# Performance work log

Hardware: AMD Instinct MI355X
Metric: run time of the kernel (lower is better)

## Reference

```python
import jax, jax.numpy as jnp
import numpy as np

DIM = 384
HEAD_DIM = 32
NUM_HEADS = DIM // HEAD_DIM
SCALE = HEAD_DIM ** -0.5


def setup_inputs() -> dict:
    key = jax.random.key(0)
    k1, k2, k3, k4 = jax.random.split(key, 4)
    x = jax.random.normal(k1, (8, DIM, 32, 32), dtype=jnp.float32)
    # torch nn.Linear stores weight as [out_features, in_features]
    W_qkv = jax.random.normal(k2, (3 * DIM, DIM), dtype=jnp.float32) * (DIM ** -0.5)
    W_proj = jax.random.normal(k3, (DIM, DIM), dtype=jnp.float32) * (DIM ** -0.5)
    b_proj = jax.random.normal(k4, (DIM,), dtype=jnp.float32) * 0.01
    return {"x": x, "W_qkv": W_qkv, "W_proj": W_proj, "b_proj": b_proj}


def reference(x, W_qkv, W_proj, b_proj):
    B, C, H, W = x.shape
    N = H * W
    # flatten spatial -> tokens: (B, N, C)
    xt = x.reshape(B, C, N).transpose(0, 2, 1)
    # qkv projection (no bias): (B, N, 3C)
    qkv = jnp.einsum('bnc,oc->bno', xt, W_qkv)
    qkv = qkv.reshape(B, N, 3, NUM_HEADS, HEAD_DIM).transpose(2, 0, 3, 1, 4)
    q, k, v = qkv[0], qkv[1], qkv[2]  # each (B, h, N, d)
    attn = jnp.einsum('bhnd,bhmd->bhnm', q * SCALE, k)  # (B, h, N, N)
    attn = jax.nn.softmax(attn, axis=-1)
    out = jnp.einsum('bhnm,bhmd->bhnd', attn, v)  # (B, h, N, d)
    out = out.transpose(0, 2, 1, 3).reshape(B, N, C)
    out = jnp.einsum('bnc,oc->bno', out, W_proj) + b_proj
    # back to (B, C, H, W)
    return out.transpose(0, 2, 1).reshape(B, C, H, W)
```

## Files before the change

kernel.cpp:

```cpp
#include <hip/hip_runtime.h>
#include <hip/hip_bf16.h>

#define DIM   384
#define HD    32
#define NH    12
#define NT    1024
#define BATCH 8
#define C2 0.2550347244197545f
#define M2 11.541560327111707f


typedef short shortx8 __attribute__((ext_vector_type(8)));
typedef float floatx4 __attribute__((ext_vector_type(4)));

#define GLD_LDS(gp, lp) \
    __builtin_amdgcn_global_load_lds((__attribute__((address_space(1))) const void*)(gp), \
                                     (__attribute__((address_space(3))) void*)(lp), 16, 0, 0)

static __device__ __forceinline__ unsigned short f2bf(float f) {
    unsigned int u = __float_as_uint(f);
    u += 0x7fffu + ((u >> 16) & 1u);
    return (unsigned short)(u >> 16);
}

template <int NA, int NB>
static __device__ __forceinline__ void ldfrag(shortx8 (&A)[NA], shortx8 (&B)[NB],
                                              const unsigned short* ab,
                                              const unsigned short* bb, int ks) {
#pragma unroll
    for (int s = 0; s < NA; s++) A[s] = *(const shortx8*)(ab + s * 6144 + ks * 512);
#pragma unroll
    for (int s = 0; s < NB; s++) B[s] = *(const shortx8*)(bb + s * 6144 + ks * 512);
}
template <int NA, int NB>
static __device__ __forceinline__ void mmblk(floatx4 (&acc)[NA][NB],
                                             const shortx8 (&A)[NA], const shortx8 (&B)[NB]) {
#pragma unroll
    for (int sm = 0; sm < NA; sm++)
#pragma unroll
        for (int sn = 0; sn < NB; sn++)
            acc[sm][sn] = __builtin_amdgcn_mfma_f32_16x16x32_bf16(A[sm], B[sn], acc[sm][sn], 0, 0, 0);
}

__global__ __launch_bounds__(256) void k_pre(const float* __restrict__ x,
                                             const float* __restrict__ wq,
                                             const float* __restrict__ wp,
                                             unsigned short* __restrict__ xtf,
                                             unsigned short* __restrict__ wqf,
                                             unsigned short* __restrict__ wpf) {
    const int bid = blockIdx.x;
    if (bid < 3072) {
        __shared__ float t[32][33];
        const int xb_ = bid & 31, kstep = (bid >> 5) % 12, b = bid / 384;
        const int n0 = xb_ * 32;
        const int tid = threadIdx.x;
        const int row = tid >> 3, col4 = (tid & 7) * 4;
        const float* xb = x + ((size_t)b * DIM + kstep * 32) * NT + n0;
        const float4 v4 = *(const float4*)(xb + (size_t)row * NT + col4);
        t[row][col4 + 0] = v4.x;
        t[row][col4 + 1] = v4.y;
        t[row][col4 + 2] = v4.z;
        t[row][col4 + 3] = v4.w;
        __syncthreads();
        const int mtl = tid >> 7, kq = (tid >> 5) & 3, rem = tid & 31;
        const int mrow = rem >> 1, krH = rem & 1;
        ushort4 p;
        p.x = f2bf(t[kq * 8 + krH * 4 + 0][mtl * 16 + mrow]);
        p.y = f2bf(t[kq * 8 + krH * 4 + 1][mtl * 16 + mrow]);
        p.z = f2bf(t[kq * 8 + krH * 4 + 2][mtl * 16 + mrow]);
        p.w = f2bf(t[kq * 8 + krH * 4 + 3][mtl * 16 + mrow]);
        const size_t mtile = ((size_t)b * 1024 + n0) / 16 + mtl;
        const size_t off = ((mtile * 12 + kstep) * 4 + kq) * 128 + mrow * 8 + krH * 4;
        *(ushort4*)(xtf + off) = p;
    } else {
        const int tid = (bid - 3072) * 256 + threadIdx.x;
        const float* src; unsigned short* dst; int ci;
        if (tid < 110592) { ci = tid; src = wq; dst = wqf; }
        else              { ci = tid - 110592; src = wp; dst = wpf; }
        const int krH = ci & 1, orow = (ci >> 1) & 15, quad = (ci >> 5) & 3;
        const int t2 = ci >> 7, kstep = t2 % 12, ntile = t2 / 12;
        const int row = ntile * 16 + orow, col = kstep * 32 + quad * 8 + krH * 4;
        const float4 v = *(const float4*)(src + (size_t)row * DIM + col);
        ushort4 p;
        p.x = f2bf(v.x); p.y = f2bf(v.y); p.z = f2bf(v.z); p.w = f2bf(v.w);
        *(ushort4*)(dst + (size_t)ci * 4) = p;
    }
}

__global__ __launch_bounds__(256, 6) void k_qkv(const unsigned short* __restrict__ xtf,
                                                const unsigned short* __restrict__ wqf,
                                                unsigned short* __restrict__ qb,
                                                unsigned short* __restrict__ kvf) {
    const int lane = threadIdx.x & 63, w = threadIdx.x >> 6;
    const int quad = lane >> 4, l16 = lane & 15;
    const int m0 = blockIdx.x * 64 + (w & 1) * 32;
    const int n0 = blockIdx.y * 96 + (w >> 1) * 48;
    floatx4 acc[2][3] = {};
    const unsigned short* abase = xtf + ((size_t)(m0 >> 4) * 48 + quad) * 128 + l16 * 8;
    const unsigned short* bbase = wqf + ((size_t)(n0 >> 4) * 48 + quad) * 128 + l16 * 8;
    shortx8 A0[2], B0[3], A1[2], B1[3];
    ldfrag(A0, B0, abase, bbase, 0);
#pragma unroll
    for (int ks = 0; ks < 12; ks += 2) {
        if (ks + 1 < 12) ldfrag(A1, B1, abase, bbase, ks + 1);
        mmblk(acc, A0, B0);
        if (ks + 2 < 12) ldfrag(A0, B0, abase, bbase, ks + 2);
        mmblk(acc, A1, B1);
    }
    const int bi = m0 >> 10;
#pragma unroll
    for (int sn = 0; sn < 3; sn++) {
        const int o = n0 + sn * 16 + l16;
        const int which = (o >= 2 * DIM) ? 2 : (o >= DIM ? 1 : 0);
        const int rem = o - which * DIM;
        const int h = rem >> 5, d = rem & 31;
        const size_t hi = (size_t)bi * NH + h;
#pragma unroll
        for (int sm = 0; sm < 2; sm++) {
            if (which == 2) {
                const int nb = m0 + sm * 16 + quad * 4;
                const int n_ = nb & 1023;
                const int f = 2 + (d >> 4);
                const int ln = (d & 15) + 16 * ((n_ & 31) >> 3);
                ushort4 p;
                p.x = f2bf(acc[sm][sn][0]);
                p.y = f2bf(acc[sm][sn][1]);
                p.z = f2bf(acc[sm][sn][2]);
                p.w = f2bf(acc[sm][sn][3]);
                *(ushort4*)(kvf + ((hi * 32 + (n_ >> 5)) * 4 + f) * 512 + ln * 8 + (n_ & 7)) = p;
            } else {
#pragma unroll
                for (int r = 0; r < 4; r++) {
                    const int n = (m0 + sm * 16 + quad * 4 + r) & 1023;
                    const unsigned short val = f2bf(acc[sm][sn][r]);
                    if (which == 0) {
                        qb[(hi * NT + n) * HD + d] = val;
                    } else {
                        const int key = n & 31;
                        const int kf_ = ((key & 7) < 4) ? 0 : 1;
                        const int kk = key - 4 * kf_;
                        const int l16p = ((kk >> 3) << 2) | (kk & 3);
                        const int pos = (l16p + 16 * (d >> 3)) * 8 + (d & 7);
                        kvf[((hi * 32 + (n >> 5)) * 4 + kf_) * 512 + pos] = val;
                    }
                }
            }
        }
    }
}

__global__ __launch_bounds__(256, 6) void k_attn(const unsigned short* __restrict__ qb,
                                                 const unsigned short* __restrict__ kvf,
                                                 unsigned short* __restrict__ aoutf) {
    __shared__ __align__(16) unsigned short frag[2][2][4][512];
    const int lane = threadIdx.x & 63, w = threadIdx.x >> 6;
    const int quad = lane >> 4, l16 = lane & 15;
    const int g = blockIdx.x & 7, j = blockIdx.x >> 3;
    const int hi = g * 12 + j % 12;
    const int q0 = (j / 12) * 64 + w * 16;
    const unsigned short* Q = qb + (size_t)hi * NT * HD;

    const shortx8 qf = *(const shortx8*)(Q + (size_t)(q0 + l16) * HD + quad * 8);
    const unsigned short* gsrc = kvf + ((size_t)hi * 32 * 4 + w) * 512 + lane * 8;
    const int gstep = 4 * 512;

    const shortx8 ones = {16256, 16256, 16256, 16256, 16256, 16256, 16256, 16256};
    floatx4 olo = {}, ohi = {}, ds = {};
    const floatx4 zero = {};

#pragma unroll
    for (int t = 0; t < 2; t++)
        GLD_LDS(gsrc + (size_t)t * gstep, &frag[0][t][w][0]);
    __syncthreads();

    for (int p = 0; p < 16; p++) {
        const int pb = p & 1;
        if (p < 15) {
#pragma unroll
            for (int t = 0; t < 2; t++)
                GLD_LDS(gsrc + (size_t)((p + 1) * 2 + t) * gstep, &frag[pb ^ 1][t][w][0]);
        }
#pragma unroll
        for (int t = 0; t < 2; t++) {
            const unsigned short* fb = &frag[pb][t][0][0];
            const shortx8 kf0 = *(const shortx8*)(fb + 0 * 512 + lane * 8);
            const shortx8 kf1 = *(const shortx8*)(fb + 1 * 512 + lane * 8);
            const shortx8 vlo = *(const shortx8*)(fb + 2 * 512 + lane * 8);
            const shortx8 vhi = *(const shortx8*)(fb + 3 * 512 + lane * 8);
            const floatx4 s0 = __builtin_amdgcn_mfma_f32_16x16x32_bf16(kf0, qf, zero, 0, 0, 0);
            const floatx4 s1 = __builtin_amdgcn_mfma_f32_16x16x32_bf16(kf1, qf, zero, 0, 0, 0);
            float e[8];
#pragma unroll
            for (int r = 0; r < 4; r++) {
                e[r]     = __builtin_amdgcn_exp2f(fmaf(s0[r], C2, -M2));
                e[4 + r] = __builtin_amdgcn_exp2f(fmaf(s1[r], C2, -M2));
            }
            union { shortx8 s8; __hip_bfloat162 h[4]; } pk;
#pragma unroll
            for (int i = 0; i < 4; i++)
                pk.h[i] = __float22bfloat162_rn(make_float2(e[2 * i], e[2 * i + 1]));
            olo = __builtin_amdgcn_mfma_f32_16x16x32_bf16(pk.s8, vlo, olo, 0, 0, 0);
            ohi = __builtin_amdgcn_mfma_f32_16x16x32_bf16(pk.s8, vhi, ohi, 0, 0, 0);
            ds  = __builtin_amdgcn_mfma_f32_16x16x32_bf16(pk.s8, ones, ds, 0, 0, 0);
        }
        __syncthreads();
    }
    const int bi = hi / NH, h = hi % NH;
    const size_t mt0 = (size_t)bi * 64 + (q0 >> 4);
    const int kqlo = l16 >> 3, kr = l16 & 7;
    unsigned short* pp = aoutf + (mt0 * 12 + h) * 512 + kr;
#pragma unroll
    for (int r = 0; r < 4; r++) {
        const int mrow8 = (quad * 4 + r) * 8;
        const float inv = 1.0f / ds[r];
        pp[kqlo * 128 + mrow8]       = f2bf(olo[r] * inv);
        pp[(2 + kqlo) * 128 + mrow8] = f2bf(ohi[r] * inv);
    }
}

__global__ __launch_bounds__(256, 6) void k_proj(const unsigned short* __restrict__ aoutf,
                                                 const unsigned short* __restrict__ wpf,
                                                 const float* __restrict__ bias,
                                                 float* __restrict__ out) {
    const int lane = threadIdx.x & 63, w = threadIdx.x >> 6;
    const int quad = lane >> 4, l16 = lane & 15;
    const int m0 = blockIdx.x * 32 + (w & 1) * 16;
    const int n0 = blockIdx.y * 64 + (w >> 1) * 32;
    floatx4 acc[1][2] = {};
    const unsigned short* abase = aoutf + ((size_t)(m0 >> 4) * 48 + quad) * 128 + l16 * 8;
    const unsigned short* bbase = wpf + ((size_t)(n0 >> 4) * 48 + quad) * 128 + l16 * 8;
    shortx8 A0[1], B0[2], A1[1], B1[2];
    ldfrag(A0, B0, abase, bbase, 0);
#pragma unroll
    for (int ks = 0; ks < 12; ks += 2) {
        if (ks + 1 < 12) ldfrag(A1, B1, abase, bbase, ks + 1);
        mmblk(acc, A0, B0);
        if (ks + 2 < 12) ldfrag(A0, B0, abase, bbase, ks + 2);
        mmblk(acc, A1, B1);
    }
    const int bi = m0 >> 10;
#pragma unroll
    for (int sn = 0; sn < 2; sn++) {
        const int o = n0 + sn * 16 + l16;
        const float bv = bias[o];
        float* orow = out + ((size_t)bi * DIM + o) * NT;
        const int nb = (m0 + quad * 4) & 1023;
        float4 pack;
        pack.x = acc[0][sn][0] + bv;
        pack.y = acc[0][sn][1] + bv;
        pack.z = acc[0][sn][2] + bv;
        pack.w = acc[0][sn][3] + bv;
        *(float4*)(orow + nb) = pack;
    }
}

extern "C" void kernel_launch(void* const* d_in, const int* in_sizes, int n_in,
                              void* d_out, int out_size, void* d_ws, size_t ws_size,
                              hipStream_t stream) {
    const float* x     = (const float*)d_in[0];
    const float* wqkv  = (const float*)d_in[1];
    const float* wproj = (const float*)d_in[2];
    const float* bias  = (const float*)d_in[3];
    float* out = (float*)d_out;

    unsigned short* xtf  = (unsigned short*)d_ws;
    unsigned short* qb   = xtf + 3145728;
    unsigned short* kvf  = qb + 3145728;
    unsigned short* wqf  = kvf + 6291456;
    unsigned short* wpf  = wqf + 442368;
    unsigned short* aoutf = xtf;

    k_pre<<<3648, 256, 0, stream>>>(x, wqkv, wproj, xtf, wqf, wpf);
    k_qkv<<<dim3(128, 12), 256, 0, stream>>>(xtf, wqf, qb, kvf);
    k_attn<<<1536, 256, 0, stream>>>(qb, kvf, aoutf);
    k_proj<<<dim3(256, 6), 256, 0, stream>>>(aoutf, wpf, bias, out);
}
```

Baseline: 124.2 us.

## Fuse fp32-to-bf16 conversion into QKV and projection GEMMs, drop pre-pass kernel

```diff
diff --git a/kernel.cpp b/kernel.cpp
--- a/kernel.cpp
+++ b/kernel.cpp
@@ -23,126 +23,105 @@
     return (unsigned short)(u >> 16);
 }
 
-template <int NA, int NB>
-static __device__ __forceinline__ void ldfrag(shortx8 (&A)[NA], shortx8 (&B)[NB],
-                                              const unsigned short* ab,
-                                              const unsigned short* bb, int ks) {
-#pragma unroll
-    for (int s = 0; s < NA; s++) A[s] = *(const shortx8*)(ab + s * 6144 + ks * 512);
-#pragma unroll
-    for (int s = 0; s < NB; s++) B[s] = *(const shortx8*)(bb + s * 6144 + ks * 512);
-}
-template <int NA, int NB>
-static __device__ __forceinline__ void mmblk(floatx4 (&acc)[NA][NB],
-                                             const shortx8 (&A)[NA], const shortx8 (&B)[NB]) {
-#pragma unroll
-    for (int sm = 0; sm < NA; sm++)
-#pragma unroll
-        for (int sn = 0; sn < NB; sn++)
-            acc[sm][sn] = __builtin_amdgcn_mfma_f32_16x16x32_bf16(A[sm], B[sn], acc[sm][sn], 0, 0, 0);
-}
-
-__global__ __launch_bounds__(256) void k_pre(const float* __restrict__ x,
-                                             const float* __restrict__ wq,
-                                             const float* __restrict__ wp,
-                                             unsigned short* __restrict__ xtf,
-                                             unsigned short* __restrict__ wqf,
-                                             unsigned short* __restrict__ wpf) {
-    const int bid = blockIdx.x;
-    if (bid < 3072) {
-        __shared__ float t[32][33];
-        const int xb_ = bid & 31, kstep = (bid >> 5) % 12, b = bid / 384;
-        const int n0 = xb_ * 32;
-        const int tid = threadIdx.x;
-        const int row = tid >> 3, col4 = (tid & 7) * 4;
-        const float* xb = x + ((size_t)b * DIM + kstep * 32) * NT + n0;
-        const float4 v4 = *(const float4*)(xb + (size_t)row * NT + col4);
-        t[row][col4 + 0] = v4.x;
-        t[row][col4 + 1] = v4.y;
-        t[row][col4 + 2] = v4.z;
-        t[row][col4 + 3] = v4.w;
-        __syncthreads();
-        const int mtl = tid >> 7, kq = (tid >> 5) & 3, rem = tid & 31;
-        const int mrow = rem >> 1, krH = rem & 1;
-        ushort4 p;
-        p.x = f2bf(t[kq * 8 + krH * 4 + 0][mtl * 16 + mrow]);
-        p.y = f2bf(t[kq * 8 + krH * 4 + 1][mtl * 16 + mrow]);
-        p.z = f2bf(t[kq * 8 + krH * 4 + 2][mtl * 16 + mrow]);
-        p.w = f2bf(t[kq * 8 + krH * 4 + 3][mtl * 16 + mrow]);
-        const size_t mtile = ((size_t)b * 1024 + n0) / 16 + mtl;
-        const size_t off = ((mtile * 12 + kstep) * 4 + kq) * 128 + mrow * 8 + krH * 4;
-        *(ushort4*)(xtf + off) = p;
-    } else {
-        const int tid = (bid - 3072) * 256 + threadIdx.x;
-        const float* src; unsigned short* dst; int ci;
-        if (tid < 110592) { ci = tid; src = wq; dst = wqf; }
-        else              { ci = tid - 110592; src = wp; dst = wpf; }
-        const int krH = ci & 1, orow = (ci >> 1) & 15, quad = (ci >> 5) & 3;
-        const int t2 = ci >> 7, kstep = t2 % 12, ntile = t2 / 12;
-        const int row = ntile * 16 + orow, col = kstep * 32 + quad * 8 + krH * 4;
-        const float4 v = *(const float4*)(src + (size_t)row * DIM + col);
-        ushort4 p;
-        p.x = f2bf(v.x); p.y = f2bf(v.y); p.z = f2bf(v.z); p.w = f2bf(v.w);
-        *(ushort4*)(dst + (size_t)ci * 4) = p;
-    }
-}
-
-__global__ __launch_bounds__(256, 6) void k_qkv(const unsigned short* __restrict__ xtf,
-                                                const unsigned short* __restrict__ wqf,
+static __device__ __forceinline__ shortx8 ldw(const float* __restrict__ p) {
+    const float4 a = *(const float4*)p;
+    const float4 b = *(const float4*)(p + 4);
+    union { shortx8 s8; __hip_bfloat162 h[4]; } u;
+    u.h[0] = __float22bfloat162_rn(make_float2(a.x, a.y));
+    u.h[1] = __float22bfloat162_rn(make_float2(a.z, a.w));
+    u.h[2] = __float22bfloat162_rn(make_float2(b.x, b.y));
+    u.h[3] = __float22bfloat162_rn(make_float2(b.z, b.w));
+    return u.s8;
+}
+
+__global__ __launch_bounds__(256, 4) void k_qkv(const float* __restrict__ x,
+                                                const float* __restrict__ wq,
                                                 unsigned short* __restrict__ qb,
                                                 unsigned short* __restrict__ kvf) {
-    const int lane = threadIdx.x & 63, w = threadIdx.x >> 6;
+    __shared__ __align__(16) unsigned short afrag[2][12][4][128];
+    const int tid = threadIdx.x;
+    const int lane = tid & 63, w = tid >> 6;
     const int quad = lane >> 4, l16 = lane & 15;
-    const int m0 = blockIdx.x * 64 + (w & 1) * 32;
+    const int sb = blockIdx.x;
+    const int b = sb >> 5;
+    {
+        const int n_ = tid & 31, cg = tid >> 5;
+        const float* xsrc = x + ((size_t)b * DIM + cg * 4) * NT + (sb & 31) * 32 + n_;
+        unsigned short* ldst = &afrag[n_ >> 4][0][cg >> 1][(n_ & 15) * 8 + (cg & 1) * 4];
+#pragma unroll
+        for (int ks = 0; ks < 12; ks++) {
+            ushort4 p;
+            p.x = f2bf(xsrc[(size_t)(ks * 32 + 0) * NT]);
+            p.y = f2bf(xsrc[(size_t)(ks * 32 + 1) * NT]);
+            p.z = f2bf(xsrc[(size_t)(ks * 32 + 2) * NT]);
+            p.w = f2bf(xsrc[(size_t)(ks * 32 + 3) * NT]);
+            *(ushort4*)(ldst + ks * 512) = p;
+        }
+    }
+    __syncthreads();
+    const int mt = w & 1;
     const int n0 = blockIdx.y * 96 + (w >> 1) * 48;
-    floatx4 acc[2][3] = {};
-    const unsigned short* abase = xtf + ((size_t)(m0 >> 4) * 48 + quad) * 128 + l16 * 8;
-    const unsigned short* bbase = wqf + ((size_t)(n0 >> 4) * 48 + quad) * 128 + l16 * 8;
-    shortx8 A0[2], B0[3], A1[2], B1[3];
-    ldfrag(A0, B0, abase, bbase, 0);
+    const unsigned short* abase = &afrag[mt][0][quad][l16 * 8];
+    const float* wrow[3];
+#pragma unroll
+    for (int s = 0; s < 3; s++)
+        wrow[s] = wq + (size_t)(n0 + s * 16 + l16) * DIM + quad * 8;
+    floatx4 acc[3] = {};
+    shortx8 A0, A1, B0[3], B1[3];
+    A0 = *(const shortx8*)(abase);
+#pragma unroll
+    for (int s = 0; s < 3; s++) B0[s] = ldw(wrow[s]);
 #pragma unroll
     for (int ks = 0; ks < 12; ks += 2) {
-        if (ks + 1 < 12) ldfrag(A1, B1, abase, bbase, ks + 1);
-        mmblk(acc, A0, B0);
-        if (ks + 2 < 12) ldfrag(A0, B0, abase, bbase, ks + 2);
-        mmblk(acc, A1, B1);
-    }
-    const int bi = m0 >> 10;
+        if (ks + 1 < 12) {
+            A1 = *(const shortx8*)(abase + (ks + 1) * 512);
+#pragma unroll
+            for (int s = 0; s < 3; s++) B1[s] = ldw(wrow[s] + (ks + 1) * 32);
+        }
+#pragma unroll
+        for (int s = 0; s < 3; s++)
+            acc[s] = __builtin_amdgcn_mfma_f32_16x16x32_bf16(A0, B0[s], acc[s], 0, 0, 0);
+        if (ks + 2 < 12) {
+            A0 = *(const shortx8*)(abase + (ks + 2) * 512);
+#pragma unroll
+            for (int s = 0; s < 3; s++) B0[s] = ldw(wrow[s] + (ks + 2) * 32);
+        }
+#pragma unroll
+        for (int s = 0; s < 3; s++)
+            acc[s] = __builtin_amdgcn_mfma_f32_16x16x32_bf16(A1, B1[s], acc[s], 0, 0, 0);
+    }
+    const int m0w = sb * 32 + mt * 16;
 #pragma unroll
     for (int sn = 0; sn < 3; sn++) {
         const int o = n0 + sn * 16 + l16;
         const int which = (o >= 2 * DIM) ? 2 : (o >= DIM ? 1 : 0);
         const int rem = o - which * DIM;
         const int h = rem >> 5, d = rem & 31;
-        const size_t hi = (size_t)bi * NH + h;
-#pragma unroll
-        for (int sm = 0; sm < 2; sm++) {
-            if (which == 2) {
-                const int nb = m0 + sm * 16 + quad * 4;
-                const int n_ = nb & 1023;
-                const int f = 2 + (d >> 4);
-                const int ln = (d & 15) + 16 * ((n_ & 31) >> 3);
-                ushort4 p;
-                p.x = f2bf(acc[sm][sn][0]);
-                p.y = f2bf(acc[sm][sn][1]);
-                p.z = f2bf(acc[sm][sn][2]);
-                p.w = f2bf(acc[sm][sn][3]);
-                *(ushort4*)(kvf + ((hi * 32 + (n_ >> 5)) * 4 + f) * 512 + ln * 8 + (n_ & 7)) = p;
-            } else {
-#pragma unroll
-                for (int r = 0; r < 4; r++) {
-                    const int n = (m0 + sm * 16 + quad * 4 + r) & 1023;
-                    const unsigned short val = f2bf(acc[sm][sn][r]);
-                    if (which == 0) {
-                        qb[(hi * NT + n) * HD + d] = val;
-                    } else {
-                        const int key = n & 31;
-                        const int kf_ = ((key & 7) < 4) ? 0 : 1;
-                        const int kk = key - 4 * kf_;
-                        const int l16p = ((kk >> 3) << 2) | (kk & 3);
-                        const int pos = (l16p + 16 * (d >> 3)) * 8 + (d & 7);
-                        kvf[((hi * 32 + (n >> 5)) * 4 + kf_) * 512 + pos] = val;
-                    }
+        const size_t hi = (size_t)b * NH + h;
+        if (which == 2) {
+            const int n_ = (m0w + quad * 4) & 1023;
+            const int f = 2 + (d >> 4);
+            const int ln = (d & 15) + 16 * ((n_ & 31) >> 3);
+            ushort4 p;
+            p.x = f2bf(acc[sn][0]);
+            p.y = f2bf(acc[sn][1]);
+            p.z = f2bf(acc[sn][2]);
+            p.w = f2bf(acc[sn][3]);
+            *(ushort4*)(kvf + ((hi * 32 + (n_ >> 5)) * 4 + f) * 512 + ln * 8 + (n_ & 7)) = p;
+        } else {
+#pragma unroll
+            for (int r = 0; r < 4; r++) {
+                const int n = (m0w + quad * 4 + r) & 1023;
+                const unsigned short val = f2bf(acc[sn][r]);
+                if (which == 0) {
+                    qb[(hi * NT + n) * HD + d] = val;
+                } else {
+                    const int key = n & 31;
+                    const int kf_ = ((key & 7) < 4) ? 0 : 1;
+                    const int kk = key - 4 * kf_;
+                    const int l16p = ((kk >> 3) << 2) | (kk & 3);
+                    const int pos = (l16p + 16 * (d >> 3)) * 8 + (d & 7);
+                    kvf[((hi * 32 + (n >> 5)) * 4 + kf_) * 512 + pos] = val;
                 }
             }
         }
@@ -218,38 +197,55 @@
     }
 }
 
-__global__ __launch_bounds__(256, 6) void k_proj(const unsigned short* __restrict__ aoutf,
-                                                 const unsigned short* __restrict__ wpf,
+__global__ __launch_bounds__(256, 4) void k_proj(const unsigned short* __restrict__ aoutf,
+                                                 const float* __restrict__ wp,
                                                  const float* __restrict__ bias,
                                                  float* __restrict__ out) {
     const int lane = threadIdx.x & 63, w = threadIdx.x >> 6;
     const int quad = lane >> 4, l16 = lane & 15;
     const int m0 = blockIdx.x * 32 + (w & 1) * 16;
-    const int n0 = blockIdx.y * 64 + (w >> 1) * 32;
-    floatx4 acc[1][2] = {};
+    const int n0 = blockIdx.y * 96 + (w >> 1) * 48;
     const unsigned short* abase = aoutf + ((size_t)(m0 >> 4) * 48 + quad) * 128 + l16 * 8;
-    const unsigned short* bbase = wpf + ((size_t)(n0 >> 4) * 48 + quad) * 128 + l16 * 8;
-    shortx8 A0[1], B0[2], A1[1], B1[2];
-    ldfrag(A0, B0, abase, bbase, 0);
+    const float* wrow[3];
+#pragma unroll
+    for (int s = 0; s < 3; s++)
+        wrow[s] = wp + (size_t)(n0 + s * 16 + l16) * DIM + quad * 8;
+    floatx4 acc[3] = {};
+    shortx8 A0, A1, B0[3], B1[3];
+    A0 = *(const shortx8*)(abase);
+#pragma unroll
+    for (int s = 0; s < 3; s++) B0[s] = ldw(wrow[s]);
 #pragma unroll
     for (int ks = 0; ks < 12; ks += 2) {
-        if (ks + 1 < 12) ldfrag(A1, B1, abase, bbase, ks + 1);
-        mmblk(acc, A0, B0);
-        if (ks + 2 < 12) ldfrag(A0, B0, abase, bbase, ks + 2);
-        mmblk(acc, A1, B1);
+        if (ks + 1 < 12) {
+            A1 = *(const shortx8*)(abase + (ks + 1) * 512);
+#pragma unroll
+            for (int s = 0; s < 3; s++) B1[s] = ldw(wrow[s] + (ks + 1) * 32);
+        }
+#pragma unroll
+        for (int s = 0; s < 3; s++)
+            acc[s] = __builtin_amdgcn_mfma_f32_16x16x32_bf16(A0, B0[s], acc[s], 0, 0, 0);
+        if (ks + 2 < 12) {
+            A0 = *(const shortx8*)(abase + (ks + 2) * 512);
+#pragma unroll
+            for (int s = 0; s < 3; s++) B0[s] = ldw(wrow[s] + (ks + 2) * 32);
+        }
+#pragma unroll
+        for (int s = 0; s < 3; s++)
+            acc[s] = __builtin_amdgcn_mfma_f32_16x16x32_bf16(A1, B1[s], acc[s], 0, 0, 0);
     }
     const int bi = m0 >> 10;
 #pragma unroll
-    for (int sn = 0; sn < 2; sn++) {
+    for (int sn = 0; sn < 3; sn++) {
         const int o = n0 + sn * 16 + l16;
         const float bv = bias[o];
         float* orow = out + ((size_t)bi * DIM + o) * NT;
         const int nb = (m0 + quad * 4) & 1023;
         float4 pack;
-        pack.x = acc[0][sn][0] + bv;
-        pack.y = acc[0][sn][1] + bv;
-        pack.z = acc[0][sn][2] + bv;
-        pack.w = acc[0][sn][3] + bv;
+        pack.x = acc[sn][0] + bv;
+        pack.y = acc[sn][1] + bv;
+        pack.z = acc[sn][2] + bv;
+        pack.w = acc[sn][3] + bv;
         *(float4*)(orow + nb) = pack;
     }
 }
@@ -263,15 +259,11 @@
     const float* bias  = (const float*)d_in[3];
     float* out = (float*)d_out;
 
-    unsigned short* xtf  = (unsigned short*)d_ws;
-    unsigned short* qb   = xtf + 3145728;
-    unsigned short* kvf  = qb + 3145728;
-    unsigned short* wqf  = kvf + 6291456;
-    unsigned short* wpf  = wqf + 442368;
-    unsigned short* aoutf = xtf;
-
-    k_pre<<<3648, 256, 0, stream>>>(x, wqkv, wproj, xtf, wqf, wpf);
-    k_qkv<<<dim3(128, 12), 256, 0, stream>>>(xtf, wqf, qb, kvf);
+    unsigned short* qb    = (unsigned short*)d_ws;
+    unsigned short* kvf   = qb + 3145728;
+    unsigned short* aoutf = kvf + 6291456;
+
+    k_qkv<<<dim3(256, 12), 256, 0, stream>>>(x, wqkv, qb, kvf);
     k_attn<<<1536, 256, 0, stream>>>(qb, kvf, aoutf);
-    k_proj<<<dim3(256, 6), 256, 0, stream>>>(aoutf, wpf, bias, out);
-}
+    k_proj<<<dim3(256, 4), 256, 0, stream>>>(aoutf, wproj, bias, out);
+}
```

Result: slower. 223.9 us (+80.2%).
